# Performance work log

Measured on AMD Instinct MI355X. Metric: run time of the kernel, lower is better.

The kernel has to match this reference:

```python
import jax, jax.numpy as jnp
import numpy as np


def _parallel_scan_affine(log_a, b):
    """Hillis-Steele doubling scan for h_t = a_t*h_{t-1} + b_t (h_0 = 0).

    log_a, b: (B, T, d). Operator: (la2,b2) o (la1,b1) = (la1+la2, exp(la2)*b1 + b2).
    """
    T = log_a.shape[1]
    la, bv = log_a, b
    stride = 1
    while stride < T:  # static Python loop, log2(T) rounds
        la_prev = jnp.roll(la, stride, axis=1).at[:, :stride, :].set(0.0)
        bv_prev = jnp.roll(bv, stride, axis=1).at[:, :stride, :].set(0.0)
        bv = jnp.exp(la) * bv_prev + bv
        la = la + la_prev
        stride *= 2
    return bv


def setup_inputs() -> dict:
    key = jax.random.key(0)
    kx, kwz, kwh = jax.random.split(key, 3)
    B, T, D = 4, 4096, 1024
    x = jax.random.normal(kx, (B, T, D), dtype=jnp.float32)
    # nn.Linear(D, D) weights, stored as (out, in) like torch
    Wz = jax.random.normal(kwz, (D, D), dtype=jnp.float32) * 0.02
    bz = jnp.zeros((D,), dtype=jnp.float32)
    Wh = jax.random.normal(kwh, (D, D), dtype=jnp.float32) * 0.02
    bh = jnp.zeros((D,), dtype=jnp.float32)
    return {"x": x, "Wz": Wz, "bz": bz, "Wh": Wh, "bh": bh}


def reference(x, Wz, bz, Wh, bh):
    # forward_parallel: z = sigmoid(linear_z(x)); h_tilde = linear_h(x)
    z = jax.nn.sigmoid(jnp.einsum("btd,ed->bte", x, Wz) + bz)
    h_tilde = jnp.einsum("btd,ed->bte", x, Wh) + bh
    log_a = jnp.log(1.0 - z + 1e-08)
    b = z * h_tilde
    h_out = _parallel_scan_affine(log_a, b)
    return h_out  # out_proj is Identity since d_inner == d_model
```

## Files before the change

### kernel.cpp

```cpp
#include <hip/hip_runtime.h>
#include <hip/hip_bf16.h>


typedef __bf16 bf16x8 __attribute__((ext_vector_type(8)));
typedef __bf16 bf16x4 __attribute__((ext_vector_type(4)));
typedef float  f32x4  __attribute__((ext_vector_type(4)));

#define BSZ 4
#define TSZ 4096
#define DSZ 1024
#define MSZ (BSZ*TSZ)
#define CH  32
#define NC  (TSZ/CH)

__device__ __forceinline__ void gload_lds16(const __bf16* g, __bf16* l) {
  __builtin_amdgcn_global_load_lds(
      (const __attribute__((address_space(1))) void*)g,
      (__attribute__((address_space(3))) void*)l, 16, 0, 0);
}

__global__ __launch_bounds__(256) void convert_tile_kernel(
    const float* __restrict__ X, const float* __restrict__ Wz,
    const float* __restrict__ Wh,
    __bf16* __restrict__ Xc, __bf16* __restrict__ Wzc, __bf16* __restrict__ Whc)
{
  __shared__ __align__(16) __bf16 T[128*40];
  const int bx = blockIdx.x;
  const float* src; __bf16* dst; int tile;
  if (bx < 4096)      { src = X;  dst = Xc;  tile = bx; }
  else if (bx < 4352) { src = Wz; dst = Wzc; tile = bx - 4096; }
  else                { src = Wh; dst = Whc; tile = bx - 4352; }
  const int rowblk = tile >> 5;
  const int kblk   = tile & 31;
  const int t = threadIdx.x;
  #pragma unroll
  for (int rr = 0; rr < 4; ++rr) {
    const int flat = rr*256 + t;
    const int r    = flat >> 3;
    const int c4   = (flat & 7) * 4;
    float4 v = *(const float4*)(src + (size_t)(rowblk*128 + r)*DSZ + kblk*32 + c4);
    bf16x4 p; p[0]=(__bf16)v.x; p[1]=(__bf16)v.y; p[2]=(__bf16)v.z; p[3]=(__bf16)v.w;
    *(bf16x4*)(T + r*40 + c4) = p;
  }
  __syncthreads();
  #pragma unroll
  for (int half = 0; half < 2; ++half) {
    const int f   = half*2048 + t*8;
    const int i   = f >> 9;
    const int l   = (f >> 3) & 63;
    const int row = i*16 + (l & 15);
    const int k   = (l >> 4) * 8;
    bf16x8 p = *(const bf16x8*)(T + row*40 + k);
    *(bf16x8*)(dst + (size_t)tile*4096 + f) = p;
  }
}

__global__ __launch_bounds__(256, 2) void gemm_gate_kernel(
    const __bf16* __restrict__ Xc,  const __bf16* __restrict__ Wzc,
    const __bf16* __restrict__ Whc,
    const float* __restrict__ bz, const float* __restrict__ bh,
    __bf16* __restrict__ a_ws, float* __restrict__ b_out,
    float* __restrict__ Aprod, float* __restrict__ Bcomp)
{
  __shared__ __align__(16) __bf16 Bzs[4096];
  __shared__ __align__(16) __bf16 Bhs[4096];

  const int tid  = threadIdx.x;
  const int lane = tid & 63;
  const int wv   = tid >> 6;
  const int wM   = (wv >> 1) * 64;
  const int wN   = (wv & 1) * 64;
  const int wMg  = wM >> 4;
  const int wNg  = wN >> 4;
  const int lr   = lane & 15;
  const int q    = lane >> 4;
  const int wbase = wv * 64;

  const int Nb = blockIdx.x;
  const int Mb = blockIdx.y;
  const __bf16* Xb = Xc  + (size_t)Mb * 32 * 4096;
  const __bf16* Zb = Wzc + (size_t)Nb * 32 * 4096;
  const __bf16* Hb = Whc + (size_t)Nb * 32 * 4096;

  f32x4 accz[4][4] = {};
  f32x4 acch[4][4] = {};

  for (int kblk = 0; kblk < 32; ++kblk) {
    __syncthreads();
    const size_t tb = (size_t)kblk * 4096;
    #pragma unroll
    for (int c = 0; c < 2; ++c) {
      const int eo = (c*256 + wbase + lane) * 8;
      const int lo = (c*256 + wbase) * 8;
      gload_lds16(Zb + tb + eo, Bzs + lo);
      gload_lds16(Hb + tb + eo, Bhs + lo);
    }
    bf16x8 af[4];
    #pragma unroll
    for (int i = 0; i < 4; ++i)
      af[i] = *(const bf16x8*)(Xb + tb + (size_t)(wMg + i)*512 + lane*8);
    __syncthreads();

    #pragma unroll
    for (int j = 0; j < 4; ++j) {
      bf16x8 bz8 = *(const bf16x8*)(Bzs + (wNg + j)*512 + lane*8);
      bf16x8 bh8 = *(const bf16x8*)(Bhs + (wNg + j)*512 + lane*8);
      #pragma unroll
      for (int i = 0; i < 4; ++i) {
        accz[j][i] = __builtin_amdgcn_mfma_f32_16x16x32_bf16(af[i], bz8, accz[j][i], 0, 0, 0);
        acch[j][i] = __builtin_amdgcn_mfma_f32_16x16x32_bf16(af[i], bh8, acch[j][i], 0, 0, 0);
      }
    }
  }

  const int M0 = Mb * 128;
  const int N0 = Nb * 128;
  #pragma unroll
  for (int j = 0; j < 4; ++j) {
    const int e = N0 + wN + j*16 + lr;
    const float bzv = bz[e];
    const float bhv = bh[e];
    float Aseg[4], Bseg[4];
    #pragma unroll
    for (int i = 0; i < 4; ++i) {
      const int mbase = M0 + wM + i*16 + q*4;
      float A = 1.0f, Bv = 0.0f;
      #pragma unroll
      for (int r = 0; r < 4; ++r) {
        const size_t idx = (size_t)(mbase + r)*DSZ + e;
        const float pz = accz[j][i][r] + bzv;
        const float ph = acch[j][i][r] + bhv;
        const float ex = __expf(-pz);
        const float z  = 1.0f / (1.0f + ex);
        const __bf16 abf = (__bf16)fmaf(ex, z, 1e-8f);
        const float  af2 = (float)abf;
        const float  bf2 = z * ph;
        a_ws[idx]  = abf;
        b_out[idx] = bf2;
        Bv = fmaf(af2, Bv, bf2);
        A *= af2;
      }
      Aseg[i] = A; Bseg[i] = Bv;
    }
    #pragma unroll
    for (int i = 0; i < 4; ++i) {
      #pragma unroll
      for (int s = 16; s < 64; s <<= 1) {
        const float Ap = __shfl_up(Aseg[i], s, 64);
        const float Bp = __shfl_up(Bseg[i], s, 64);
        if (lane >= s) { Bseg[i] = fmaf(Aseg[i], Bp, Bseg[i]); Aseg[i] *= Ap; }
      }
    }
    if (q == 3) {
      #pragma unroll
      for (int c = 0; c < 2; ++c) {
        const float Ac = Aseg[2*c+1] * Aseg[2*c];
        const float Bc = fmaf(Aseg[2*c+1], Bseg[2*c], Bseg[2*c+1]);
        const int bc = (M0 + wM + c*32) >> 5;
        Aprod[(size_t)bc*DSZ + e] = Ac;
        Bcomp[(size_t)bc*DSZ + e] = Bc;
      }
    }
  }
}

__global__ void scan_pass2_kernel(const float* __restrict__ Aprod,
                                  const float* __restrict__ Bcomp,
                                  float* __restrict__ Hstart)
{
  const int lane = threadIdx.x & 63;
  const int wave = (blockIdx.x * 256 + threadIdx.x) >> 6;
  const int b = wave >> 10;
  const int d = wave & 1023;
  const size_t i0 = (size_t)(b*NC + 2*lane)*DSZ + d;
  const float A0 = Aprod[i0],       B0 = Bcomp[i0];
  const float A1 = Aprod[i0 + DSZ], B1 = Bcomp[i0 + DSZ];
  float A  = A0 * A1;
  float Bv = fmaf(A1, B0, B1);
  #pragma unroll
  for (int s = 1; s < 64; s <<= 1) {
    const float Ap = __shfl_up(A,  s, 64);
    const float Bp = __shfl_up(Bv, s, 64);
    if (lane >= s) { Bv = fmaf(A, Bp, Bv); A *= Ap; }
  }
  float Hp = __shfl_up(Bv, 1, 64);
  if (lane == 0) Hp = 0.0f;
  Hstart[i0]       = Hp;
  Hstart[i0 + DSZ] = fmaf(A0, Hp, B0);
}

__global__ void scan_pass3_kernel(const __bf16* __restrict__ a_ws,
                                  const float* __restrict__ Hstart,
                                  float* __restrict__ out)
{
  const int bc   = blockIdx.x;
  const int d0   = threadIdx.x * 4;
  const size_t base = (size_t)bc * CH * DSZ + d0;
  float4 hv = *(const float4*)(Hstart + (size_t)bc*DSZ + d0);
  float h[4] = {hv.x, hv.y, hv.z, hv.w};
  #pragma unroll 8
  for (int t = 0; t < CH; ++t) {
    bf16x4 a4 = *(const bf16x4*)(a_ws + base + (size_t)t*DSZ);
    float4 b4 = *(const float4*)(out + base + (size_t)t*DSZ);
    const float bb[4] = {b4.x, b4.y, b4.z, b4.w};
    #pragma unroll
    for (int c = 0; c < 4; ++c)
      h[c] = fmaf((float)a4[c], h[c], bb[c]);
    *(float4*)(out + base + (size_t)t*DSZ) = make_float4(h[0], h[1], h[2], h[3]);
  }
}

extern "C" void kernel_launch(void* const* d_in, const int* in_sizes, int n_in,
                              void* d_out, int out_size, void* d_ws, size_t ws_size,
                              hipStream_t stream)
{
  const float* x  = (const float*)d_in[0];
  const float* Wz = (const float*)d_in[1];
  const float* bz = (const float*)d_in[2];
  const float* Wh = (const float*)d_in[3];
  const float* bh = (const float*)d_in[4];
  float* out = (float*)d_out;

  __bf16* Xc   = (__bf16*)d_ws;
  __bf16* Wzc  = Xc  + (size_t)MSZ * DSZ;
  __bf16* Whc  = Wzc + (size_t)DSZ * DSZ;
  __bf16* a_ws = Whc + (size_t)DSZ * DSZ;
  float* Aprod  = (float*)(a_ws + (size_t)MSZ * DSZ);
  float* Bcomp  = Aprod + (size_t)BSZ*NC*DSZ;
  float* Hstart = Bcomp + (size_t)BSZ*NC*DSZ;

  convert_tile_kernel<<<4608, 256, 0, stream>>>(x, Wz, Wh, Xc, Wzc, Whc);
  gemm_gate_kernel<<<dim3(8, 128), 256, 0, stream>>>(
      Xc, Wzc, Whc, bz, bh, a_ws, out, Aprod, Bcomp);
  scan_pass2_kernel<<<(BSZ*DSZ)/4, 256, 0, stream>>>(Aprod, Bcomp, Hstart);
  scan_pass3_kernel<<<BSZ*NC, 256, 0, stream>>>(a_ws, Hstart, out);
}
```

Measured before the change: 244.8 us.

## Fuse X bf16 conversion into GEMM and pack a,b as bf16 pairs

The separate X-to-bf16 conversion pass is dropped: the GEMM now reads fp32 X directly, converts it in registers and stages it in a new LDS tile. The gate outputs a and b are stored as packed bf16 pairs in one 32-bit word instead of bf16 a plus fp32 b written into the output, which cuts intermediate traffic in the final scan pass. The grid is remapped to a 1D swizzle for L2 locality across M blocks sharing the same N block. In exchange, each N-block re-reads and re-converts X (8x fp32 reads of X), and b loses precision by being rounded to bf16.

```diff
diff --git a/kernel.cpp b/kernel.cpp
--- a/kernel.cpp
+++ b/kernel.cpp
@@ -19,17 +19,15 @@
       (__attribute__((address_space(3))) void*)l, 16, 0, 0);
 }
 
-__global__ __launch_bounds__(256) void convert_tile_kernel(
-    const float* __restrict__ X, const float* __restrict__ Wz,
-    const float* __restrict__ Wh,
-    __bf16* __restrict__ Xc, __bf16* __restrict__ Wzc, __bf16* __restrict__ Whc)
+__global__ __launch_bounds__(256) void convert_w_kernel(
+    const float* __restrict__ Wz, const float* __restrict__ Wh,
+    __bf16* __restrict__ Wzc, __bf16* __restrict__ Whc)
 {
   __shared__ __align__(16) __bf16 T[128*40];
   const int bx = blockIdx.x;
   const float* src; __bf16* dst; int tile;
-  if (bx < 4096)      { src = X;  dst = Xc;  tile = bx; }
-  else if (bx < 4352) { src = Wz; dst = Wzc; tile = bx - 4096; }
-  else                { src = Wh; dst = Whc; tile = bx - 4352; }
+  if (bx < 256) { src = Wz; dst = Wzc; tile = bx; }
+  else          { src = Wh; dst = Whc; tile = bx - 256; }
   const int rowblk = tile >> 5;
   const int kblk   = tile & 31;
   const int t = threadIdx.x;
@@ -56,12 +54,13 @@
 }
 
 __global__ __launch_bounds__(256, 2) void gemm_gate_kernel(
-    const __bf16* __restrict__ Xc,  const __bf16* __restrict__ Wzc,
-    const __bf16* __restrict__ Whc,
+    const float* __restrict__ X,
+    const __bf16* __restrict__ Wzc, const __bf16* __restrict__ Whc,
     const float* __restrict__ bz, const float* __restrict__ bh,
-    __bf16* __restrict__ a_ws, float* __restrict__ b_out,
+    unsigned int* __restrict__ AB,
     float* __restrict__ Aprod, float* __restrict__ Bcomp)
 {
+  __shared__ __align__(16) __bf16 As [4096];
   __shared__ __align__(16) __bf16 Bzs[4096];
   __shared__ __align__(16) __bf16 Bhs[4096];
 
@@ -76,9 +75,14 @@
   const int q    = lane >> 4;
   const int wbase = wv * 64;
 
-  const int Nb = blockIdx.x;
-  const int Mb = blockIdx.y;
-  const __bf16* Xb = Xc  + (size_t)Mb * 32 * 4096;
+  const int f  = blockIdx.x;
+  const int x  = f & 7;
+  const int g  = f >> 3;
+  const int Nb = g & 7;
+  const int Mb = (g >> 3) * 8 + x;
+  const int M0 = Mb * 128;
+  const int N0 = Nb * 128;
+
   const __bf16* Zb = Wzc + (size_t)Nb * 32 * 4096;
   const __bf16* Hb = Whc + (size_t)Nb * 32 * 4096;
 
@@ -95,12 +99,27 @@
       gload_lds16(Zb + tb + eo, Bzs + lo);
       gload_lds16(Hb + tb + eo, Bhs + lo);
     }
+    #pragma unroll
+    for (int c = 0; c < 2; ++c) {
+      const int o   = c*256 + tid;
+      const int ii  = o >> 6;
+      const int ll  = o & 63;
+      const int row = M0 + ii*16 + (ll & 15);
+      const int kk  = kblk*32 + (ll >> 4)*8;
+      const float* gp = X + (size_t)row*DSZ + kk;
+      float4 v0 = *(const float4*)gp;
+      float4 v1 = *(const float4*)(gp + 4);
+      bf16x8 p;
+      p[0]=(__bf16)v0.x; p[1]=(__bf16)v0.y; p[2]=(__bf16)v0.z; p[3]=(__bf16)v0.w;
+      p[4]=(__bf16)v1.x; p[5]=(__bf16)v1.y; p[6]=(__bf16)v1.z; p[7]=(__bf16)v1.w;
+      *(bf16x8*)(As + o*8) = p;
+    }
+    __syncthreads();
+
     bf16x8 af[4];
     #pragma unroll
     for (int i = 0; i < 4; ++i)
-      af[i] = *(const bf16x8*)(Xb + tb + (size_t)(wMg + i)*512 + lane*8);
-    __syncthreads();
-
+      af[i] = *(const bf16x8*)(As + (wMg + i)*512 + lane*8);
     #pragma unroll
     for (int j = 0; j < 4; ++j) {
       bf16x8 bz8 = *(const bf16x8*)(Bzs + (wNg + j)*512 + lane*8);
@@ -113,8 +132,6 @@
     }
   }
 
-  const int M0 = Mb * 128;
-  const int N0 = Nb * 128;
   #pragma unroll
   for (int j = 0; j < 4; ++j) {
     const int e = N0 + wN + j*16 + lr;
@@ -133,12 +150,14 @@
         const float ex = __expf(-pz);
         const float z  = 1.0f / (1.0f + ex);
         const __bf16 abf = (__bf16)fmaf(ex, z, 1e-8f);
-        const float  af2 = (float)abf;
-        const float  bf2 = z * ph;
-        a_ws[idx]  = abf;
-        b_out[idx] = bf2;
-        Bv = fmaf(af2, Bv, bf2);
-        A *= af2;
+        const __bf16 bbf = (__bf16)(z * ph);
+        const unsigned int au = __builtin_bit_cast(unsigned short, abf);
+        const unsigned int bu = __builtin_bit_cast(unsigned short, bbf);
+        AB[idx] = au | (bu << 16);
+        const float afv = __uint_as_float(au << 16);
+        const float bfv = __uint_as_float(bu << 16);
+        Bv = fmaf(afv, Bv, bfv);
+        A *= afv;
       }
       Aseg[i] = A; Bseg[i] = Bv;
     }
@@ -189,24 +208,26 @@
   Hstart[i0 + DSZ] = fmaf(A0, Hp, B0);
 }
 
-__global__ void scan_pass3_kernel(const __bf16* __restrict__ a_ws,
+__global__ void scan_pass3_kernel(const unsigned int* __restrict__ AB,
                                   const float* __restrict__ Hstart,
                                   float* __restrict__ out)
 {
-  const int bc   = blockIdx.x;
-  const int d0   = threadIdx.x * 4;
+  const int bc   = blockIdx.x >> 1;
+  const int half = blockIdx.x & 1;
+  const int d0   = half*512 + threadIdx.x*2;
   const size_t base = (size_t)bc * CH * DSZ + d0;
-  float4 hv = *(const float4*)(Hstart + (size_t)bc*DSZ + d0);
-  float h[4] = {hv.x, hv.y, hv.z, hv.w};
+  float2 hv = *(const float2*)(Hstart + (size_t)bc*DSZ + d0);
+  float h0 = hv.x, h1 = hv.y;
   #pragma unroll 8
   for (int t = 0; t < CH; ++t) {
-    bf16x4 a4 = *(const bf16x4*)(a_ws + base + (size_t)t*DSZ);
-    float4 b4 = *(const float4*)(out + base + (size_t)t*DSZ);
-    const float bb[4] = {b4.x, b4.y, b4.z, b4.w};
-    #pragma unroll
-    for (int c = 0; c < 4; ++c)
-      h[c] = fmaf((float)a4[c], h[c], bb[c]);
-    *(float4*)(out + base + (size_t)t*DSZ) = make_float4(h[0], h[1], h[2], h[3]);
+    const uint2 p = *(const uint2*)(AB + base + (size_t)t*DSZ);
+    const float a0 = __uint_as_float((p.x & 0xffffu) << 16);
+    const float b0 = __uint_as_float(p.x & 0xffff0000u);
+    const float a1 = __uint_as_float((p.y & 0xffffu) << 16);
+    const float b1 = __uint_as_float(p.y & 0xffff0000u);
+    h0 = fmaf(a0, h0, b0);
+    h1 = fmaf(a1, h1, b1);
+    *(float2*)(out + base + (size_t)t*DSZ) = make_float2(h0, h1);
   }
 }
 
@@ -221,17 +242,15 @@
   const float* bh = (const float*)d_in[4];
   float* out = (float*)d_out;
 
-  __bf16* Xc   = (__bf16*)d_ws;
-  __bf16* Wzc  = Xc  + (size_t)MSZ * DSZ;
+  __bf16* Wzc  = (__bf16*)d_ws;
   __bf16* Whc  = Wzc + (size_t)DSZ * DSZ;
-  __bf16* a_ws = Whc + (size_t)DSZ * DSZ;
-  float* Aprod  = (float*)(a_ws + (size_t)MSZ * DSZ);
+  unsigned int* AB = (unsigned int*)(Whc + (size_t)DSZ * DSZ);
+  float* Aprod  = (float*)(AB + (size_t)MSZ * DSZ);
   float* Bcomp  = Aprod + (size_t)BSZ*NC*DSZ;
   float* Hstart = Bcomp + (size_t)BSZ*NC*DSZ;
 
-  convert_tile_kernel<<<4608, 256, 0, stream>>>(x, Wz, Wh, Xc, Wzc, Whc);
-  gemm_gate_kernel<<<dim3(8, 128), 256, 0, stream>>>(
-      Xc, Wzc, Whc, bz, bh, a_ws, out, Aprod, Bcomp);
+  convert_w_kernel<<<512, 256, 0, stream>>>(Wz, Wh, Wzc, Whc);
+  gemm_gate_kernel<<<1024, 256, 0, stream>>>(x, Wzc, Whc, bz, bh, AB, Aprod, Bcomp);
   scan_pass2_kernel<<<(BSZ*DSZ)/4, 256, 0, stream>>>(Aprod, Bcomp, Hstart);
-  scan_pass3_kernel<<<BSZ*NC, 256, 0, stream>>>(a_ws, Hstart, out);
-}
+  scan_pass3_kernel<<<BSZ*NC*2, 256, 0, stream>>>(AB, Hstart, out);
+}
```

After: 267.1 us. 1.09x slower.
